# Optimization experiments

Hardware: AMD Instinct MI355X
Metric: run time of the kernel (lower is better)

The kernel has to match this reference:

```python
import jax, jax.numpy as jnp
import numpy as np

H = 64  # LSTM hidden size per direction


def _lstm_dir(x, Wih, Whh, b, reverse):
    # x: [B,T,I]; Wih: [4H,I]; Whh: [4H,H]; b: [4H] (b_ih + b_hh combined)
    if reverse:
        x = x[:, ::-1]
    xg = jnp.einsum('bti,gi->btg', x, Wih) + b  # precompute input gates [B,T,4H]
    B = x.shape[0]
    WhhT = Whh.T  # [H,4H]

    def step(carry, xt_g):
        h, c = carry
        g = xt_g + h @ WhhT  # [B,4H]
        i, f, gg, o = jnp.split(g, 4, axis=-1)  # PyTorch gate order i,f,g,o
        c = jax.nn.sigmoid(f) * c + jax.nn.sigmoid(i) * jnp.tanh(gg)
        h = jax.nn.sigmoid(o) * jnp.tanh(c)
        return (h, c), h

    h0 = jnp.zeros((B, H), x.dtype)
    _, hs = jax.lax.scan(step, (h0, h0), jnp.swapaxes(xg, 0, 1))
    hs = jnp.swapaxes(hs, 0, 1)  # [B,T,H]
    if reverse:
        hs = hs[:, ::-1]
    return hs


def _bilstm(x, wih_f, whh_f, b_f, wih_b, whh_b, b_b):
    fwd = _lstm_dir(x, wih_f, whh_f, b_f, False)
    bwd = _lstm_dir(x, wih_b, whh_b, b_b, True)
    return jnp.concatenate([fwd, bwd], axis=-1)  # [B,T,2H]


def setup_inputs() -> dict:
    key = jax.random.key(0)
    ks = jax.random.split(key, 16)
    B, IN = 8192, 20

    def w(k, shape, fan_in):
        return jax.random.normal(k, shape, jnp.float32) * (1.0 / np.sqrt(fan_in))

    inp = {
        'x': jax.random.normal(ks[0], (B, IN), jnp.float32),
        'fc1_w': w(ks[1], (50, IN), IN),
        'fc1_b': jnp.zeros((50,), jnp.float32),
        # rnn1: input_size=1, bidirectional
        'r1_wih_f': w(ks[2], (4 * H, 1), 1),
        'r1_whh_f': w(ks[3], (4 * H, H), H),
        'r1_b_f': jnp.zeros((4 * H,), jnp.float32),
        'r1_wih_b': w(ks[4], (4 * H, 1), 1),
        'r1_whh_b': w(ks[5], (4 * H, H), H),
        'r1_b_b': jnp.zeros((4 * H,), jnp.float32),
        # rnn2: input_size=2H=128, bidirectional
        'r2_wih_f': w(ks[6], (4 * H, 2 * H), 2 * H),
        'r2_whh_f': w(ks[7], (4 * H, H), H),
        'r2_b_f': jnp.zeros((4 * H,), jnp.float32),
        'r2_wih_b': w(ks[8], (4 * H, 2 * H), 2 * H),
        'r2_whh_b': w(ks[9], (4 * H, H), H),
        'r2_b_b': jnp.zeros((4 * H,), jnp.float32),
        'fc2_w': w(ks[10], (1, 2 * H), 2 * H),
        'fc2_b': jnp.zeros((1,), jnp.float32),
    }
    return inp


def reference(x, fc1_w, fc1_b,
              r1_wih_f, r1_whh_f, r1_b_f, r1_wih_b, r1_whh_b, r1_b_b,
              r2_wih_f, r2_whh_f, r2_b_f, r2_wih_b, r2_whh_b, r2_b_b,
              fc2_w, fc2_b):
    h = x @ fc1_w.T + fc1_b            # [B,50]
    h = h[..., None]                   # [B,50,1]
    h = _bilstm(h, r1_wih_f, r1_whh_f, r1_b_f, r1_wih_b, r1_whh_b, r1_b_b)  # [B,50,128]
    h = jnp.repeat(h, 2, axis=1)       # nearest upsample x2 along time -> [B,100,128]
    h = _bilstm(h, r2_wih_f, r2_whh_f, r2_b_f, r2_wih_b, r2_whh_b, r2_b_b)  # [B,100,128]
    out = jnp.tanh(jnp.einsum('btf,of->bto', h, fc2_w) + fc2_b)  # [B,100,1]
    return out
```

## Files before the change

### kernel.cpp

```cpp
#include <hip/hip_runtime.h>
#include <cmath>

#define H1    64
#define T1    50
#define T2    100
#define BATCH 8192
#define NB2   256
#define NTILE 512

typedef __attribute__((ext_vector_type(8))) short s16x8;
typedef __attribute__((ext_vector_type(4))) float f32x4;

#define MFMA16(a,b,c) __builtin_amdgcn_mfma_f32_16x16x32_bf16(a,b,c,0,0,0)

#define S_SIG  (-1.4426950408889634f)
#define S_TANH ( 2.8853900817779268f)

#define OFF_FC1T  ((size_t)0)
#define OFF_XF    ((size_t)1638400)
#define OFF_WA1   ((size_t)(1638400 + 104857600))
#define OFF_WA2HH (OFF_WA1 + 65536)
#define OFF_WA2IH (OFF_WA2HH + 65536)
#define OFF_PART  (OFF_WA2IH + 131072)
#define OFF_BS    (OFF_PART + 6553600)

__device__ __forceinline__ float rcp_(float x) { return __builtin_amdgcn_rcpf(x); }
__device__ __forceinline__ float exp2_(float x) {
#if __has_builtin(__builtin_amdgcn_exp2f)
    return __builtin_amdgcn_exp2f(x);
#else
    return exp2f(x);
#endif
}
__device__ __forceinline__ float sigp_(float e)  { return rcp_(1.f + exp2_(e)); }
__device__ __forceinline__ float tanhp_(float e) { return 1.f - 2.f * rcp_(1.f + exp2_(e)); }
__device__ __forceinline__ float tanhc_(float c) { return tanhp_(S_TANH * c); }
__device__ __forceinline__ float tanh_(float x)  { return tanhc_(x); }

__device__ __forceinline__ unsigned short bf16_rne(float x) {
    unsigned int u = __float_as_uint(x);
    u += 0x7fffu + ((u >> 16) & 1u);
    return (unsigned short)(u >> 16);
}
__device__ __forceinline__ float bf16f(unsigned short h) {
    return __uint_as_float(((unsigned int)h) << 16);
}

__global__ __launch_bounds__(256) void k_pre(
    const float* __restrict__ whh1f, const float* __restrict__ whh1b,
    const float* __restrict__ whh2f, const float* __restrict__ whh2b,
    const float* __restrict__ wih2f, const float* __restrict__ wih2b,
    const float* __restrict__ b2f,   const float* __restrict__ b2b,
    const float* __restrict__ x, const float* __restrict__ fc1w,
    const float* __restrict__ fc1b,
    unsigned short* __restrict__ WA1, unsigned short* __restrict__ WA2HH,
    unsigned short* __restrict__ WA2IH, float* __restrict__ fc1T,
    float* __restrict__ part, float* __restrict__ BS)
{
    __shared__ float wls[1000];
    __shared__ float bls[50];
    int tid = threadIdx.x;
    int blk = blockIdx.x;
    if (blk < 64) {
        int i = blk * 256 + tid;
        if (i < 8192) {
            int a   = i >> 12;
            int r   = i & 4095;
            int dir = r >> 11, rem = r & 2047;
            int mt  = rem >> 7, rem2 = rem & 127;
            int kk  = rem2 >> 6, l = rem2 & 63;
            const float* s_ = a ? (dir ? whh2b : whh2f) : (dir ? whh1b : whh1f);
            unsigned short* d_ = a ? WA2HH : WA1;
            int gate = mt * 16 + (l & 15);
            float sc = ((gate >> 6) == 2) ? S_TANH : S_SIG;
            int k0   = kk * 32 + (l >> 4) * 8;
            const float* p = s_ + gate * 64 + k0;
            unsigned short* q = d_ + (size_t)r * 8;
#pragma unroll
            for (int j = 0; j < 8; ++j) q[j] = bf16_rne(p[j] * sc);
        } else {
            int r   = i - 8192;
            int dir = r >> 12, rem = r & 4095;
            int mt  = rem >> 8, rem2 = rem & 255;
            int kk  = rem2 >> 6, l = rem2 & 63;
            const float* s_ = dir ? wih2b : wih2f;
            int gate = mt * 16 + (l & 15);
            float sc = ((gate >> 6) == 2) ? S_TANH : S_SIG;
            int k0   = kk * 32 + (l >> 4) * 8;
            const float* p = s_ + gate * 128 + k0;
            unsigned short* q = WA2IH + (size_t)r * 8;
#pragma unroll
            for (int j = 0; j < 8; ++j) q[j] = bf16_rne(p[j] * sc);
        }
    } else if (blk < 96) {
        for (int i = tid; i < 1000; i += 256) wls[i] = fc1w[i];
        if (tid < 50) bls[tid] = fc1b[tid];
        __syncthreads();
        int bidx = (blk - 64) * 256 + tid;
        float xv[20];
#pragma unroll
        for (int i = 0; i < 20; ++i) xv[i] = x[bidx * 20 + i];
        for (int t = 0; t < T1; ++t) {
            float s = bls[t];
#pragma unroll
            for (int i = 0; i < 20; ++i) s += xv[i] * wls[t * 20 + i];
            fc1T[t * BATCH + bidx] = s;
        }
    } else if (blk < 352) {
        const int n = 2 * T2 * BATCH;
        for (int i = (blk - 96) * 256 + tid; i < n; i += 256 * 256) part[i] = 0.f;
    } else {
        for (int i = tid; i < 512; i += 256) {
            int d = i >> 8, m = i & 255;
            const float* bb = d ? b2b : b2f;
            float sc = ((m >> 6) == 2) ? S_TANH : S_SIG;
            BS[i] = bb[m] * sc;
        }
    }
}

__global__ __launch_bounds__(512, 4) void k_lstm1(
    const float* __restrict__ wih1f, const float* __restrict__ b1f,
    const float* __restrict__ wih1b, const float* __restrict__ b1b,
    const unsigned short* __restrict__ WA1,
    const float* __restrict__ fc1T,
    unsigned short* __restrict__ XF)
{
    __shared__ float x1s[T1][32];
    __shared__ unsigned short Htf[2][2][2][2][64][8];
    int tid  = threadIdx.x;
    int lane = tid & 63;
    int w    = __builtin_amdgcn_readfirstlane(tid >> 6);
    int wh   = w & 3, wsh = w >> 2;
    int quad = lane >> 4, col = lane & 15;
    int dir  = blockIdx.y, bblk = blockIdx.x;

    for (int i = tid; i < T1 * 32; i += 512) {
        int t = i >> 5, s = i & 31;
        x1s[t][s] = fc1T[t * BATCH + bblk * 32 + s];
    }
    const float* wih = dir ? wih1b : wih1f;
    const float* bia = dir ? b1b : b1f;
    f32x4 wvv[4], bvv[4];
#pragma unroll
    for (int g = 0; g < 4; ++g) {
        float sc = (g == 2) ? S_TANH : S_SIG;
#pragma unroll
        for (int r = 0; r < 4; ++r) {
            int gate = g * 64 + wh * 16 + quad * 4 + r;
            wvv[g][r] = wih[gate] * sc;
            bvv[g][r] = bia[gate] * sc;
        }
    }
    s16x8 whhA[4][2];
#pragma unroll
    for (int g = 0; g < 4; ++g)
#pragma unroll
        for (int kk = 0; kk < 2; ++kk)
            whhA[g][kk] = *(const s16x8*)(WA1 +
                ((size_t)((dir * 16 + (g * 4 + wh)) * 2 + kk) * 64 + lane) * 8);

    float c[4];
#pragma unroll
    for (int r = 0; r < 4; ++r) c[r] = 0.f;

    int lq  = 2 * (wh & 1) + (quad >> 1);
    int lp  = lq * 16 + col;
    int jo  = (quad & 1) * 4;
    int kkw = wh >> 1;
    int kk1 = dir * 2 + (wh >> 1);
    int gtile = bblk * 2 + wsh;
    __syncthreads();
    int buf = 0;
    for (int step = 0; step < T1; ++step) {
        int t = dir ? (T1 - 1 - step) : step;
        float xt = x1s[t][wsh * 16 + col];
        f32x4 acc[4];
#pragma unroll
        for (int g = 0; g < 4; ++g)
#pragma unroll
            for (int r = 0; r < 4; ++r)
                acc[g][r] = bvv[g][r] + wvv[g][r] * xt;
        if (step) {
#pragma unroll
            for (int hf = 0; hf < 2; ++hf) {
                s16x8 hb0 = *(const s16x8*)&Htf[buf][hf][0][wsh][lane][0];
                s16x8 hb1 = *(const s16x8*)&Htf[buf][hf][1][wsh][lane][0];
#pragma unroll
                for (int g = 0; g < 4; ++g) {
                    acc[g] = MFMA16(whhA[g][0], hb0, acc[g]);
                    acc[g] = MFMA16(whhA[g][1], hb1, acc[g]);
                }
            }
        }
        int nbuf = buf ^ 1;
        unsigned short hh[4], hl[4];
#pragma unroll
        for (int r = 0; r < 4; ++r) {
            float cc = sigp_(acc[1][r]) * c[r] + sigp_(acc[0][r]) * tanhp_(acc[2][r]);
            c[r] = cc;
            float h = sigp_(acc[3][r]) * tanhc_(cc);
            hh[r] = bf16_rne(h);
            hl[r] = bf16_rne(h - bf16f(hh[r]));
        }
        uint2 vhi, vlo;
        vhi.x = (unsigned)hh[0] | ((unsigned)hh[1] << 16);
        vhi.y = (unsigned)hh[2] | ((unsigned)hh[3] << 16);
        vlo.x = (unsigned)hl[0] | ((unsigned)hl[1] << 16);
        vlo.y = (unsigned)hl[2] | ((unsigned)hl[3] << 16);
        *(uint2*)&Htf[nbuf][0][kkw][wsh][lp][jo] = vhi;
        *(uint2*)&Htf[nbuf][1][kkw][wsh][lp][jo] = vlo;
        *(uint2*)(XF + ((((size_t)t * 4 + kk1) * NTILE + gtile) * 64 + lp) * 8 + jo) = vhi;
        __syncthreads();
        buf = nbuf;
    }
}

__global__ __launch_bounds__(512, 4) void k_lstm2(
    const float* __restrict__ BS,
    const float* __restrict__ fc2w,
    const unsigned short* __restrict__ WA2HH,
    const unsigned short* __restrict__ WA2IH,
    const unsigned short* __restrict__ XF,
    float* __restrict__ part)
{
    __shared__ unsigned short wAl[16][4][64][8];
    __shared__ unsigned short Htf[2][2][2][2][64][8];
    int tid  = threadIdx.x;
    int lane = tid & 63;
    int w    = __builtin_amdgcn_readfirstlane(tid >> 6);
    int wh   = w & 3, wsh = w >> 2;
    int quad = lane >> 4, col = lane & 15;
    int dir  = blockIdx.y, bblk = blockIdx.x;
    int gtile = bblk * 2 + wsh;

    {
        const uint4* src = (const uint4*)(WA2IH + (size_t)dir * 32768);
        uint4* dst = (uint4*)&wAl[0][0][0][0];
        for (int i = tid; i < 4096; i += 512) dst[i] = src[i];
    }
    float f2v[4];
#pragma unroll
    for (int r = 0; r < 4; ++r)
        f2v[r] = fc2w[dir * 64 + wh * 16 + quad * 4 + r];

    s16x8 whhA[4][2];
#pragma unroll
    for (int g = 0; g < 4; ++g)
#pragma unroll
        for (int kk = 0; kk < 2; ++kk)
            whhA[g][kk] = *(const s16x8*)(WA2HH +
                ((size_t)((dir * 16 + (g * 4 + wh)) * 2 + kk) * 64 + lane) * 8);

    const float4* bsp = (const float4*)(BS + dir * 256 + wh * 16 + quad * 4);

    float c[4];
#pragma unroll
    for (int r = 0; r < 4; ++r) c[r] = 0.f;

    int lq  = 2 * (wh & 1) + (quad >> 1);
    int lp  = lq * 16 + col;
    int jo  = (quad & 1) * 4;
    int kkw = wh >> 1;

    s16x8 xbC[4], xbN[4];
    {
        int tp0 = dir ? (T1 - 1) : 0;
#pragma unroll
        for (int kk = 0; kk < 4; ++kk)
            xbC[kk] = *(const s16x8*)(XF +
                (((size_t)(tp0 * 4 + kk) * NTILE + gtile) * 64 + lane) * 8);
    }
    f32x4 xacc[4];
    __syncthreads();
    int buf = 0;

    for (int step = 0; step < T2; ++step) {
        int t2 = dir ? (T2 - 1 - step) : step;
        if ((step & 1) == 0) {
#pragma unroll
            for (int g = 0; g < 4; ++g) {
                float4 bv4 = bsp[g * 16];
                f32x4 a; a[0] = bv4.x; a[1] = bv4.y; a[2] = bv4.z; a[3] = bv4.w;
#pragma unroll
                for (int kk = 0; kk < 4; ++kk) {
                    s16x8 wa = *(const s16x8*)&wAl[g * 4 + wh][kk][lane][0];
                    a = MFMA16(wa, xbC[kk], a);
                }
                xacc[g] = a;
            }
            int tp  = t2 >> 1;
            int tpn = dir ? (tp > 0 ? tp - 1 : 0) : (tp < T1 - 1 ? tp + 1 : T1 - 1);
#pragma unroll
            for (int kk = 0; kk < 4; ++kk)
                xbN[kk] = *(const s16x8*)(XF +
                    (((size_t)(tpn * 4 + kk) * NTILE + gtile) * 64 + lane) * 8);
        }
        f32x4 acc[4];
        if (step) {
            s16x8 hb00 = *(const s16x8*)&Htf[buf][0][0][wsh][lane][0];
            s16x8 hb01 = *(const s16x8*)&Htf[buf][0][1][wsh][lane][0];
            s16x8 hb10 = *(const s16x8*)&Htf[buf][1][0][wsh][lane][0];
            s16x8 hb11 = *(const s16x8*)&Htf[buf][1][1][wsh][lane][0];
#pragma unroll
            for (int g = 0; g < 4; ++g) {
                f32x4 a = MFMA16(whhA[g][0], hb00, xacc[g]);
                a = MFMA16(whhA[g][1], hb01, a);
                a = MFMA16(whhA[g][0], hb10, a);
                a = MFMA16(whhA[g][1], hb11, a);
                acc[g] = a;
            }
        } else {
#pragma unroll
            for (int g = 0; g < 4; ++g) acc[g] = xacc[g];
        }
        int nbuf = buf ^ 1;
        unsigned int uhi[4];
        unsigned short hl[4];
        float pacc = 0.f;
#pragma unroll
        for (int r = 0; r < 4; ++r) {
            float cc = sigp_(acc[1][r]) * c[r] + sigp_(acc[0][r]) * tanhp_(acc[2][r]);
            c[r] = cc;
            float h = sigp_(acc[3][r]) * tanhc_(cc);
            pacc += f2v[r] * h;
            unsigned int u = __float_as_uint(h);
            uhi[r] = u & 0xFFFF0000u;
            hl[r]  = bf16_rne(h - __uint_as_float(uhi[r]));
        }
        uint2 vhi, vlo;
        vhi.x = (uhi[0] >> 16) | uhi[1];
        vhi.y = (uhi[2] >> 16) | uhi[3];
        vlo.x = (unsigned)hl[0] | ((unsigned)hl[1] << 16);
        vlo.y = (unsigned)hl[2] | ((unsigned)hl[3] << 16);
        *(uint2*)&Htf[nbuf][0][kkw][wsh][lp][jo] = vhi;
        *(uint2*)&Htf[nbuf][1][kkw][wsh][lp][jo] = vlo;
        pacc += __shfl_xor(pacc, 16);
        pacc += __shfl_xor(pacc, 32);
        if (lane < 16)
            atomicAdd(&part[((size_t)(dir * T2 + t2)) * BATCH + bblk * 32 + wsh * 16 + lane], pacc);
        __syncthreads();
        buf = nbuf;
        if (step & 1) {
#pragma unroll
            for (int kk = 0; kk < 4; ++kk) xbC[kk] = xbN[kk];
        }
    }
}

__global__ __launch_bounds__(256) void k_fc2(const float* __restrict__ part,
                                             const float* __restrict__ fc2b,
                                             float* __restrict__ out) {
    int u = blockIdx.x * 256 + threadIdx.x;
    if (u >= BATCH * T2) return;
    int b = u / T2, t = u - b * T2;
    float p = part[(size_t)t * BATCH + b] + part[((size_t)T2 + t) * BATCH + b] + fc2b[0];
    out[u] = tanh_(p);
}

extern "C" void kernel_launch(void* const* d_in, const int* in_sizes, int n_in,
                              void* d_out, int out_size, void* d_ws, size_t ws_size,
                              hipStream_t stream) {
    const float* x      = (const float*)d_in[0];
    const float* fc1w   = (const float*)d_in[1];
    const float* fc1b   = (const float*)d_in[2];
    const float* r1wihf = (const float*)d_in[3];
    const float* r1whhf = (const float*)d_in[4];
    const float* r1bf   = (const float*)d_in[5];
    const float* r1wihb = (const float*)d_in[6];
    const float* r1whhb = (const float*)d_in[7];
    const float* r1bb   = (const float*)d_in[8];
    const float* r2wihf = (const float*)d_in[9];
    const float* r2whhf = (const float*)d_in[10];
    const float* r2bf   = (const float*)d_in[11];
    const float* r2wihb = (const float*)d_in[12];
    const float* r2whhb = (const float*)d_in[13];
    const float* r2bb   = (const float*)d_in[14];
    const float* fc2w   = (const float*)d_in[15];
    const float* fc2b   = (const float*)d_in[16];
    char* ws   = (char*)d_ws;
    float* out = (float*)d_out;

    float*          fc1T  = (float*)(ws + OFF_FC1T);
    unsigned short* XF    = (unsigned short*)(ws + OFF_XF);
    unsigned short* WA1   = (unsigned short*)(ws + OFF_WA1);
    unsigned short* WA2HH = (unsigned short*)(ws + OFF_WA2HH);
    unsigned short* WA2IH = (unsigned short*)(ws + OFF_WA2IH);
    float*          partp = (float*)(ws + OFF_PART);
    float*          BS    = (float*)(ws + OFF_BS);

    k_pre<<<353, 256, 0, stream>>>(r1whhf, r1whhb, r2whhf, r2whhb, r2wihf, r2wihb,
                                   r2bf, r2bb, x, fc1w, fc1b,
                                   WA1, WA2HH, WA2IH, fc1T, partp, BS);
    dim3 g1(NB2, 2);
    k_lstm1<<<g1, 512, 0, stream>>>(r1wihf, r1bf, r1wihb, r1bb, WA1, fc1T, XF);
    k_lstm2<<<g1, 512, 0, stream>>>(BS, fc2w, WA2HH, WA2IH, XF, partp);
    k_fc2<<<(BATCH * T2 + 255) / 256, 256, 0, stream>>>(partp, fc2b, out);
}
```

Baseline: 383.9 us.

## Unroll LSTM recurrences, fuse gate math, use packed bf16 convert and lighter barrier

```diff
diff --git a/kernel.cpp b/kernel.cpp
--- a/kernel.cpp
+++ b/kernel.cpp
@@ -42,9 +42,44 @@
     u += 0x7fffu + ((u >> 16) & 1u);
     return (unsigned short)(u >> 16);
 }
-__device__ __forceinline__ float bf16f(unsigned short h) {
-    return __uint_as_float(((unsigned int)h) << 16);
-}
+
+__device__ __forceinline__ unsigned int cvtpk_bf16(float a, float b) {
+    unsigned int r;
+    asm("v_cvt_pk_bf16_f32 %0, %1, %2" : "=v"(r) : "v"(a), "v"(b));
+    return r;
+}
+
+__device__ __forceinline__ void bar_lgkm() {
+    asm volatile("s_waitcnt lgkmcnt(0)\n\ts_barrier" ::: "memory");
+}
+
+#define CELL_PACK(ACC)                                                         \
+        float hv[4];                                                           \
+        _Pragma("unroll")                                                      \
+        for (int r = 0; r < 4; ++r) {                                          \
+            float Ei = exp2_(ACC[0][r]);                                       \
+            float Ef = exp2_(ACC[1][r]);                                       \
+            float Eg = exp2_(fminf(ACC[2][r], 100.f));                         \
+            float Eo = exp2_(ACC[3][r]);                                       \
+            float rf  = rcp_(1.f + Ef);                                        \
+            float rig = rcp_((1.f + Ei) * (1.f + Eg));                         \
+            float cc  = c4[r] * rf + (Eg - 1.f) * rig;                         \
+            c4[r] = cc;                                                        \
+            float Ec  = exp2_(fminf(S_TANH * cc, 100.f));                      \
+            float roc = rcp_((1.f + Eo) * (1.f + Ec));                         \
+            hv[r] = (Ec - 1.f) * roc;                                          \
+        }                                                                      \
+        uint2 vhi, vlo;                                                        \
+        vhi.x = cvtpk_bf16(hv[0], hv[1]);                                      \
+        vhi.y = cvtpk_bf16(hv[2], hv[3]);                                      \
+        {                                                                      \
+            float q0 = hv[0] - __uint_as_float(vhi.x << 16);                   \
+            float q1 = hv[1] - __uint_as_float(vhi.x & 0xffff0000u);           \
+            float q2 = hv[2] - __uint_as_float(vhi.y << 16);                   \
+            float q3 = hv[3] - __uint_as_float(vhi.y & 0xffff0000u);           \
+            vlo.x = cvtpk_bf16(q0, q1);                                        \
+            vlo.y = cvtpk_bf16(q2, q3);                                        \
+        }
 
 __global__ __launch_bounds__(256) void k_pre(
     const float* __restrict__ whh1f, const float* __restrict__ whh1b,
@@ -139,6 +174,11 @@
         int t = i >> 5, s = i & 31;
         x1s[t][s] = fc1T[t * BATCH + bblk * 32 + s];
     }
+    {
+        uint4* z = (uint4*)&Htf[0][0][0][0][0][0];
+        uint4 zz; zz.x = 0u; zz.y = 0u; zz.z = 0u; zz.w = 0u;
+        z[tid] = zz;
+    }
     const float* wih = dir ? wih1b : wih1f;
     const float* bia = dir ? b1b : b1f;
     f32x4 wvv[4], bvv[4];
@@ -160,60 +200,54 @@
             whhA[g][kk] = *(const s16x8*)(WA1 +
                 ((size_t)((dir * 16 + (g * 4 + wh)) * 2 + kk) * 64 + lane) * 8);
 
-    float c[4];
-#pragma unroll
-    for (int r = 0; r < 4; ++r) c[r] = 0.f;
+    float c4[4];
+#pragma unroll
+    for (int r = 0; r < 4; ++r) c4[r] = 0.f;
 
     int lq  = 2 * (wh & 1) + (quad >> 1);
     int lp  = lq * 16 + col;
     int jo  = (quad & 1) * 4;
     int kkw = wh >> 1;
-    int kk1 = dir * 2 + (wh >> 1);
+    int kk1 = dir * 2 + kkw;
     int gtile = bblk * 2 + wsh;
     __syncthreads();
-    int buf = 0;
-    for (int step = 0; step < T1; ++step) {
-        int t = dir ? (T1 - 1 - step) : step;
-        float xt = x1s[t][wsh * 16 + col];
-        f32x4 acc[4];
-#pragma unroll
-        for (int g = 0; g < 4; ++g)
-#pragma unroll
-            for (int r = 0; r < 4; ++r)
-                acc[g][r] = bvv[g][r] + wvv[g][r] * xt;
-        if (step) {
-#pragma unroll
-            for (int hf = 0; hf < 2; ++hf) {
-                s16x8 hb0 = *(const s16x8*)&Htf[buf][hf][0][wsh][lane][0];
-                s16x8 hb1 = *(const s16x8*)&Htf[buf][hf][1][wsh][lane][0];
-#pragma unroll
-                for (int g = 0; g < 4; ++g) {
-                    acc[g] = MFMA16(whhA[g][0], hb0, acc[g]);
-                    acc[g] = MFMA16(whhA[g][1], hb1, acc[g]);
-                }
-            }
-        }
-        int nbuf = buf ^ 1;
-        unsigned short hh[4], hl[4];
-#pragma unroll
-        for (int r = 0; r < 4; ++r) {
-            float cc = sigp_(acc[1][r]) * c[r] + sigp_(acc[0][r]) * tanhp_(acc[2][r]);
-            c[r] = cc;
-            float h = sigp_(acc[3][r]) * tanhc_(cc);
-            hh[r] = bf16_rne(h);
-            hl[r] = bf16_rne(h - bf16f(hh[r]));
-        }
-        uint2 vhi, vlo;
-        vhi.x = (unsigned)hh[0] | ((unsigned)hh[1] << 16);
-        vhi.y = (unsigned)hh[2] | ((unsigned)hh[3] << 16);
-        vlo.x = (unsigned)hl[0] | ((unsigned)hl[1] << 16);
-        vlo.y = (unsigned)hl[2] | ((unsigned)hl[3] << 16);
-        *(uint2*)&Htf[nbuf][0][kkw][wsh][lp][jo] = vhi;
-        *(uint2*)&Htf[nbuf][1][kkw][wsh][lp][jo] = vlo;
-        *(uint2*)(XF + ((((size_t)t * 4 + kk1) * NTILE + gtile) * 64 + lp) * 8 + jo) = vhi;
-        __syncthreads();
-        buf = nbuf;
-    }
+
+    int t = dir ? (T1 - 1) : 0;
+    const int dt = dir ? -1 : 1;
+
+#define L1_STEP(RB, WB)                                                        \
+    {                                                                          \
+        float xt = x1s[t][wsh * 16 + col];                                     \
+        f32x4 acc[4];                                                          \
+        _Pragma("unroll") for (int g = 0; g < 4; ++g)                          \
+            _Pragma("unroll") for (int r = 0; r < 4; ++r)                      \
+                acc[g][r] = bvv[g][r] + wvv[g][r] * xt;                        \
+        {                                                                      \
+            s16x8 hb00 = *(const s16x8*)&Htf[RB][0][0][wsh][lane][0];          \
+            s16x8 hb01 = *(const s16x8*)&Htf[RB][0][1][wsh][lane][0];          \
+            s16x8 hb10 = *(const s16x8*)&Htf[RB][1][0][wsh][lane][0];          \
+            s16x8 hb11 = *(const s16x8*)&Htf[RB][1][1][wsh][lane][0];          \
+            _Pragma("unroll") for (int g = 0; g < 4; ++g) {                    \
+                f32x4 a = MFMA16(whhA[g][0], hb00, acc[g]);                    \
+                a = MFMA16(whhA[g][1], hb01, a);                               \
+                a = MFMA16(whhA[g][0], hb10, a);                               \
+                a = MFMA16(whhA[g][1], hb11, a);                               \
+                acc[g] = a;                                                    \
+            }                                                                  \
+        }                                                                      \
+        CELL_PACK(acc)                                                         \
+        *(uint2*)&Htf[WB][0][kkw][wsh][lp][jo] = vhi;                          \
+        *(uint2*)&Htf[WB][1][kkw][wsh][lp][jo] = vlo;                          \
+        *(uint2*)(XF + ((((size_t)t * 4 + kk1) * NTILE + gtile) * 64 + lp) * 8 + jo) = vhi; \
+        bar_lgkm();                                                            \
+        t += dt;                                                               \
+    }
+
+    for (int it = 0; it < T1 / 2; ++it) {
+        L1_STEP(0, 1)
+        L1_STEP(1, 0)
+    }
+#undef L1_STEP
 }
 
 __global__ __launch_bounds__(512, 4) void k_lstm2(
@@ -239,6 +273,11 @@
         uint4* dst = (uint4*)&wAl[0][0][0][0];
         for (int i = tid; i < 4096; i += 512) dst[i] = src[i];
     }
+    {
+        uint4* z = (uint4*)&Htf[0][0][0][0][0][0];
+        uint4 zz; zz.x = 0u; zz.y = 0u; zz.z = 0u; zz.w = 0u;
+        z[tid] = zz;
+    }
     float f2v[4];
 #pragma unroll
     for (int r = 0; r < 4; ++r)
@@ -252,100 +291,93 @@
             whhA[g][kk] = *(const s16x8*)(WA2HH +
                 ((size_t)((dir * 16 + (g * 4 + wh)) * 2 + kk) * 64 + lane) * 8);
 
-    const float4* bsp = (const float4*)(BS + dir * 256 + wh * 16 + quad * 4);
-
-    float c[4];
-#pragma unroll
-    for (int r = 0; r < 4; ++r) c[r] = 0.f;
+    float4 bvv4[4];
+    {
+        const float* bsrc = BS + dir * 256 + wh * 16 + quad * 4;
+#pragma unroll
+        for (int g = 0; g < 4; ++g)
+            bvv4[g] = *(const float4*)(bsrc + g * 64);
+    }
+
+    float c4[4];
+#pragma unroll
+    for (int r = 0; r < 4; ++r) c4[r] = 0.f;
 
     int lq  = 2 * (wh & 1) + (quad >> 1);
     int lp  = lq * 16 + col;
     int jo  = (quad & 1) * 4;
     int kkw = wh >> 1;
 
-    s16x8 xbC[4], xbN[4];
+    s16x8 xbA[4], xbB[4];
     {
         int tp0 = dir ? (T1 - 1) : 0;
 #pragma unroll
         for (int kk = 0; kk < 4; ++kk)
-            xbC[kk] = *(const s16x8*)(XF +
+            xbA[kk] = *(const s16x8*)(XF +
                 (((size_t)(tp0 * 4 + kk) * NTILE + gtile) * 64 + lane) * 8);
     }
     f32x4 xacc[4];
     __syncthreads();
-    int buf = 0;
-
-    for (int step = 0; step < T2; ++step) {
-        int t2 = dir ? (T2 - 1 - step) : step;
-        if ((step & 1) == 0) {
-#pragma unroll
-            for (int g = 0; g < 4; ++g) {
-                float4 bv4 = bsp[g * 16];
-                f32x4 a; a[0] = bv4.x; a[1] = bv4.y; a[2] = bv4.z; a[3] = bv4.w;
-#pragma unroll
-                for (int kk = 0; kk < 4; ++kk) {
-                    s16x8 wa = *(const s16x8*)&wAl[g * 4 + wh][kk][lane][0];
-                    a = MFMA16(wa, xbC[kk], a);
-                }
-                xacc[g] = a;
-            }
-            int tp  = t2 >> 1;
-            int tpn = dir ? (tp > 0 ? tp - 1 : 0) : (tp < T1 - 1 ? tp + 1 : T1 - 1);
-#pragma unroll
-            for (int kk = 0; kk < 4; ++kk)
-                xbN[kk] = *(const s16x8*)(XF +
-                    (((size_t)(tpn * 4 + kk) * NTILE + gtile) * 64 + lane) * 8);
-        }
-        f32x4 acc[4];
-        if (step) {
-            s16x8 hb00 = *(const s16x8*)&Htf[buf][0][0][wsh][lane][0];
-            s16x8 hb01 = *(const s16x8*)&Htf[buf][0][1][wsh][lane][0];
-            s16x8 hb10 = *(const s16x8*)&Htf[buf][1][0][wsh][lane][0];
-            s16x8 hb11 = *(const s16x8*)&Htf[buf][1][1][wsh][lane][0];
-#pragma unroll
-            for (int g = 0; g < 4; ++g) {
-                f32x4 a = MFMA16(whhA[g][0], hb00, xacc[g]);
-                a = MFMA16(whhA[g][1], hb01, a);
-                a = MFMA16(whhA[g][0], hb10, a);
-                a = MFMA16(whhA[g][1], hb11, a);
-                acc[g] = a;
-            }
-        } else {
-#pragma unroll
-            for (int g = 0; g < 4; ++g) acc[g] = xacc[g];
-        }
-        int nbuf = buf ^ 1;
-        unsigned int uhi[4];
-        unsigned short hl[4];
-        float pacc = 0.f;
-#pragma unroll
-        for (int r = 0; r < 4; ++r) {
-            float cc = sigp_(acc[1][r]) * c[r] + sigp_(acc[0][r]) * tanhp_(acc[2][r]);
-            c[r] = cc;
-            float h = sigp_(acc[3][r]) * tanhc_(cc);
-            pacc += f2v[r] * h;
-            unsigned int u = __float_as_uint(h);
-            uhi[r] = u & 0xFFFF0000u;
-            hl[r]  = bf16_rne(h - __uint_as_float(uhi[r]));
-        }
-        uint2 vhi, vlo;
-        vhi.x = (uhi[0] >> 16) | uhi[1];
-        vhi.y = (uhi[2] >> 16) | uhi[3];
-        vlo.x = (unsigned)hl[0] | ((unsigned)hl[1] << 16);
-        vlo.y = (unsigned)hl[2] | ((unsigned)hl[3] << 16);
-        *(uint2*)&Htf[nbuf][0][kkw][wsh][lp][jo] = vhi;
-        *(uint2*)&Htf[nbuf][1][kkw][wsh][lp][jo] = vlo;
-        pacc += __shfl_xor(pacc, 16);
-        pacc += __shfl_xor(pacc, 32);
-        if (lane < 16)
-            atomicAdd(&part[((size_t)(dir * T2 + t2)) * BATCH + bblk * 32 + wsh * 16 + lane], pacc);
-        __syncthreads();
-        buf = nbuf;
-        if (step & 1) {
-#pragma unroll
-            for (int kk = 0; kk < 4; ++kk) xbC[kk] = xbN[kk];
-        }
-    }
+
+    int t2 = dir ? (T2 - 1) : 0;
+    const int dt = dir ? -1 : 1;
+    int tpn = dir ? (T1 - 2) : 1;
+
+#define L2_HIDCELL(RB, WB)                                                     \
+    {                                                                          \
+        s16x8 hb00 = *(const s16x8*)&Htf[RB][0][0][wsh][lane][0];              \
+        s16x8 hb01 = *(const s16x8*)&Htf[RB][0][1][wsh][lane][0];              \
+        s16x8 hb10 = *(const s16x8*)&Htf[RB][1][0][wsh][lane][0];              \
+        s16x8 hb11 = *(const s16x8*)&Htf[RB][1][1][wsh][lane][0];              \
+        f32x4 acc[4];                                                          \
+        _Pragma("unroll") for (int g = 0; g < 4; ++g) {                        \
+            f32x4 a = MFMA16(whhA[g][0], hb00, xacc[g]);                       \
+            a = MFMA16(whhA[g][1], hb01, a);                                   \
+            a = MFMA16(whhA[g][0], hb10, a);                                   \
+            a = MFMA16(whhA[g][1], hb11, a);                                   \
+            acc[g] = a;                                                        \
+        }                                                                      \
+        CELL_PACK(acc)                                                         \
+        *(uint2*)&Htf[WB][0][kkw][wsh][lp][jo] = vhi;                          \
+        *(uint2*)&Htf[WB][1][kkw][wsh][lp][jo] = vlo;                          \
+        float pacc = f2v[0]*hv[0] + f2v[1]*hv[1] + f2v[2]*hv[2] + f2v[3]*hv[3];\
+        pacc += __shfl_xor(pacc, 16);                                          \
+        pacc += __shfl_xor(pacc, 32);                                          \
+        if (lane < 16)                                                         \
+            atomicAdd(&part[((size_t)(dir * T2 + t2)) * BATCH + bblk * 32 + wsh * 16 + lane], pacc); \
+        bar_lgkm();                                                            \
+        t2 += dt;                                                              \
+    }
+
+#define L2_EVEN(XBU, XBP, RB, WB)                                              \
+    {                                                                          \
+        _Pragma("unroll") for (int g = 0; g < 4; ++g) {                        \
+            f32x4 a;                                                           \
+            a[0] = bvv4[g].x; a[1] = bvv4[g].y;                                \
+            a[2] = bvv4[g].z; a[3] = bvv4[g].w;                                \
+            _Pragma("unroll") for (int kk = 0; kk < 4; ++kk) {                 \
+                s16x8 wa = *(const s16x8*)&wAl[g * 4 + wh][kk][lane][0];       \
+                a = MFMA16(wa, XBU[kk], a);                                    \
+            }                                                                  \
+            xacc[g] = a;                                                       \
+        }                                                                      \
+        _Pragma("unroll") for (int kk = 0; kk < 4; ++kk)                       \
+            XBP[kk] = *(const s16x8*)(XF +                                     \
+                (((size_t)(tpn * 4 + kk) * NTILE + gtile) * 64 + lane) * 8);   \
+        tpn += dt;                                                             \
+        if (tpn < 0) tpn = 0;                                                  \
+        if (tpn > T1 - 1) tpn = T1 - 1;                                        \
+    }                                                                          \
+    L2_HIDCELL(RB, WB)
+
+    for (int it = 0; it < T2 / 4; ++it) {
+        L2_EVEN(xbA, xbB, 0, 1)
+        L2_HIDCELL(1, 0)
+        L2_EVEN(xbB, xbA, 0, 1)
+        L2_HIDCELL(1, 0)
+    }
+#undef L2_EVEN
+#undef L2_HIDCELL
 }
 
 __global__ __launch_bounds__(256) void k_fc2(const float* __restrict__ part,
```

After: 358.1 us. 1.07x faster.
